# Kernel optimization log

Measured on AMD Instinct MI355X. Metric: run time of the kernel, lower is better.

Reference implementation:

```python
import jax, jax.numpy as jnp
import numpy as np
from jax.scipy.special import logsumexp

B, T, N = 512, 1024, 64


def setup_inputs() -> dict:
    key = jax.random.key(0)
    k1, k2, k3, k4, k5, k6 = jax.random.split(key, 6)
    emit = jax.random.normal(k1, (B, T, N), dtype=jnp.float32)
    target = jax.random.randint(k2, (B, T), 0, N)
    # valid monotone mask: each sequence has length in [T//2, T], length >= 1
    lengths = jax.random.randint(k3, (B,), T // 2, T + 1)
    mask = jnp.arange(T)[None, :] < lengths[:, None]  # [B, T] bool
    trans = 0.1 * jax.random.normal(k4, (N, N), dtype=jnp.float32)
    strans = 0.1 * jax.random.normal(k5, (N,), dtype=jnp.float32)
    etrans = 0.1 * jax.random.normal(k6, (N,), dtype=jnp.float32)
    return {"emit": emit, "target": target, "mask": mask,
            "trans": trans, "strans": strans, "etrans": etrans}


def _get_logZ(emit_t, mask_t, trans, strans, etrans):
    # emit_t: [T, B, N], mask_t: [T, B]
    alpha0 = strans[None, :] + emit_t[0]  # [B, N]

    def step(alpha, inp):
        e_i, m_i = inp  # [B, N], [B]
        # scores[b, j] = logsumexp_i(alpha[b, i] + trans[i, j] + e_i[b, j])
        scores = logsumexp(alpha[:, :, None] + trans[None, :, :], axis=1) + e_i
        alpha = jnp.where(m_i[:, None], scores, alpha)
        return alpha, None

    alpha, _ = jax.lax.scan(step, alpha0, (emit_t[1:], mask_t[1:]))
    logZ = logsumexp(alpha + etrans[None, :], axis=1).sum()
    return logZ / B


def _get_score(emit_t, target_t, mask_t, trans, strans, etrans):
    # emit_t: [T, B, N], target_t/mask_t: [T, B]
    emit_scores = jnp.take_along_axis(emit_t, target_t[:, :, None], axis=2)[:, :, 0]  # [T, B]
    trans_scores = trans[target_t[:-1], target_t[1:]]  # [T-1, B]
    scores = emit_scores.at[1:].add(trans_scores)
    score = jnp.where(mask_t, scores, 0.0).sum()
    ends = mask_t.sum(axis=0) - 1  # [B]
    score = score + strans[target_t[0]].sum()
    last_tags = target_t[ends, jnp.arange(target_t.shape[1])]
    score = score + etrans[last_tags].sum()
    return score / B


def reference(emit, target, mask, trans, strans, etrans):
    # batch_first=True -> move to time-major [T, B, ...]
    emit_t = jnp.swapaxes(emit, 0, 1)
    target_t = target.T
    mask_t = mask.T
    logZ = _get_logZ(emit_t, mask_t, trans, strans, etrans)
    score = _get_score(emit_t, target_t, mask_t, trans, strans, etrans)
    return logZ - score
```

## Files before the change

### kernel.cpp

```cpp
#include <hip/hip_runtime.h>

#define Bn 512
#define Tn 1024
#define Nn 64
#define BURN 16

typedef float    f4  __attribute__((ext_vector_type(4)));
typedef __fp16   pk2 __attribute__((ext_vector_type(2)));
typedef __fp16   pk4 __attribute__((ext_vector_type(4)));
typedef _Float16 h8v __attribute__((ext_vector_type(8)));

__device__ __forceinline__ float wave_sum(float v) {
#pragma unroll
    for (int off = 32; off >= 1; off >>= 1) v += __shfl_xor(v, off, 64);
    return v;
}

__global__ __launch_bounds__(64) void crf_mfma(
    const float* __restrict__ emit,
    const int*   __restrict__ target,
    const int*   __restrict__ mask,
    const float* __restrict__ trans,
    const float* __restrict__ strans,
    const float* __restrict__ etrans,
    float*       __restrict__ out)
{
    __shared__ __align__(16) _Float16 plds[16 * 72];

    const int lane = threadIdx.x;
    const int n = lane & 15;
    const int g = lane >> 4;
    const int b = blockIdx.x;
    const size_t ebase = (size_t)b * Tn * Nn;

    h8v A[4][2];
#pragma unroll
    for (int r = 0; r < 4; ++r)
#pragma unroll
        for (int h = 0; h < 2; ++h) {
            h8v a;
#pragma unroll
            for (int j = 0; j < 8; ++j)
                a[j] = (_Float16)__expf(trans[(32 * h + 8 * g + j) * Nn + 16 * r + n]);
            A[r][h] = a;
        }

    const int* mrow = mask + (size_t)b * Tn;
    int lsum = 0;
#pragma unroll
    for (int k = 0; k < Tn / Nn; ++k) lsum += mrow[k * Nn + lane];
#pragma unroll
    for (int off = 32; off >= 1; off >>= 1) lsum += __shfl_xor(lsum, off, 64);
    const int len = lsum;

    const int a0    = (n * len) >> 4;
    const int a1    = ((n + 1) * len) >> 4;
    const int start = n ? (a0 - BURN) : 1;
    const int tendv = a1 - 1;
    const int maxk  = ((len + 15) >> 4) + BURN;

    float wsel[4][4];
#pragma unroll
    for (int r = 0; r < 4; ++r) {
        f4 ee = *(const f4*)(emit + ebase + (size_t)(len - 1) * Nn + 16 * r + 4 * g);
        f4 et = *(const f4*)(etrans + 16 * r + 4 * g);
#pragma unroll
        for (int c = 0; c < 4; ++c)
            wsel[r][c] = (n == 15) ? __expf(ee[c] + et[c]) : 1.0f;
    }

    float U[4][4];
#pragma unroll
    for (int r = 0; r < 4; ++r) {
        f4 st = *(const f4*)(strans + 16 * r + 4 * g);
#pragma unroll
        for (int c = 0; c < 4; ++c)
            U[r][c] = (n == 0) ? __expf(st[c]) : 1.0f;
    }

    int   S = 0;
    float L0 = 0.0f, contrib = 0.0f;

    f4 rb[4];
    {
        const int tr = start - 1;
        const f4* p = (const f4*)(emit + ebase + (size_t)tr * Nn);
#pragma unroll
        for (int r = 0; r < 4; ++r) rb[r] = p[4 * r + g];
    }
    float Wx[4][4];
#pragma unroll
    for (int r = 0; r < 4; ++r)
#pragma unroll
        for (int c = 0; c < 4; ++c) Wx[r][c] = __expf(rb[r][c]);

    const f4 zero4 = {0.f, 0.f, 0.f, 0.f};
    _Float16* myCol = plds + n * 72;

    for (int k = 0; k < maxk; ++k) {
        {
            int tr = start + k;
            if (tr > Tn - 1) tr = Tn - 1;
            const f4* p = (const f4*)(emit + ebase + (size_t)tr * Nn);
#pragma unroll
            for (int r = 0; r < 4; ++r) rb[r] = p[4 * r + g];
        }

        if (k == BURN) {
            float cs = 0.f;
#pragma unroll
            for (int r = 0; r < 4; ++r)
#pragma unroll
                for (int c = 0; c < 4; ++c) cs += U[r][c];
            cs += __shfl_xor(cs, 16, 64);
            cs += __shfl_xor(cs, 32, 64);
            float l0v = __logf(cs);
            if (n) { L0 = l0v; S = 0; }
        }

        float mx = U[0][0];
#pragma unroll
        for (int r = 0; r < 4; ++r)
#pragma unroll
            for (int c = 0; c < 4; ++c) mx = fmaxf(mx, U[r][c]);
        mx = fmaxf(mx, __shfl_xor(mx, 16, 64));
        mx = fmaxf(mx, __shfl_xor(mx, 32, 64));
        const int mk = 127 - ((__float_as_int(mx) >> 23) & 0xff);
        S += mk;

#pragma unroll
        for (int r = 0; r < 4; ++r) {
            float p0 = U[r][0] * ldexpf(Wx[r][0], mk);
            float p1 = U[r][1] * ldexpf(Wx[r][1], mk);
            float p2 = U[r][2] * ldexpf(Wx[r][2], mk);
            float p3 = U[r][3] * ldexpf(Wx[r][3], mk);
            pk2 lo = __builtin_amdgcn_cvt_pkrtz(p0, p1);
            pk2 hi = __builtin_amdgcn_cvt_pkrtz(p2, p3);
            pk4 v4 = __builtin_shufflevector(lo, hi, 0, 1, 2, 3);
            *(pk4*)&myCol[16 * r + 4 * g] = v4;
        }

        h8v B0 = *(const h8v*)&myCol[8 * g];
        h8v B1 = *(const h8v*)&myCol[32 + 8 * g];

#pragma unroll
        for (int r = 0; r < 4; ++r) {
            f4 acc = __builtin_amdgcn_mfma_f32_16x16x32_f16(A[r][0], B0, zero4, 0, 0, 0);
            acc     = __builtin_amdgcn_mfma_f32_16x16x32_f16(A[r][1], B1, acc,   0, 0, 0);
#pragma unroll
            for (int c = 0; c < 4; ++c) U[r][c] = acc[c];
        }

        bool rec = (start + k) == tendv;
        if (__any(rec)) {
            float cs = 0.f;
#pragma unroll
            for (int r = 0; r < 4; ++r)
#pragma unroll
                for (int c = 0; c < 4; ++c) cs = fmaf(U[r][c], wsel[r][c], cs);
            cs += __shfl_xor(cs, 16, 64);
            cs += __shfl_xor(cs, 32, 64);
            float lv = __logf(cs);
            if (rec) contrib = lv - (float)S * 0.6931471805599453f - L0;
        }

#pragma unroll
        for (int r = 0; r < 4; ++r)
#pragma unroll
            for (int c = 0; c < 4; ++c) Wx[r][c] = __expf(rb[r][c]);
    }

    float tot = wave_sum(contrib) * 0.25f;

    const int* trow = target + (size_t)b * Tn;
    float sc = 0.0f;
#pragma unroll
    for (int k = 0; k < Tn / Nn; ++k) {
        int t = k * Nn + lane;
        if (t < len) {
            int gT = trow[t];
            sc += emit[ebase + (size_t)t * Nn + gT];
            if (t > 0) sc += trans[trow[t - 1] * Nn + gT];
        }
    }
    sc = wave_sum(sc);

    if (lane == 0) {
        sc += strans[trow[0]] + etrans[trow[len - 1]];
        atomicAdd(out, (tot - sc) * (1.0f / (float)Bn));
    }
}

extern "C" void kernel_launch(void* const* d_in, const int* in_sizes, int n_in,
                              void* d_out, int out_size, void* d_ws, size_t ws_size,
                              hipStream_t stream) {
    const float* emit   = (const float*)d_in[0];
    const int*   target = (const int*)d_in[1];
    const int*   mask   = (const int*)d_in[2];
    const float* trans  = (const float*)d_in[3];
    const float* strans = (const float*)d_in[4];
    const float* etrans = (const float*)d_in[5];
    float* out = (float*)d_out;

    (void)hipMemsetAsync(out, 0, sizeof(float), stream);
    crf_mfma<<<Bn, Nn, 0, stream>>>(emit, target, mask, trans, strans, etrans, out);
}
```

Measured before the change: 241.6 us.

## Feed MFMA B operand from registers and deepen emit prefetch ring

```diff
diff --git a/kernel.cpp b/kernel.cpp
--- a/kernel.cpp
+++ b/kernel.cpp
@@ -8,6 +8,7 @@
 typedef float    f4  __attribute__((ext_vector_type(4)));
 typedef __fp16   pk2 __attribute__((ext_vector_type(2)));
 typedef __fp16   pk4 __attribute__((ext_vector_type(4)));
+typedef __fp16   pk8 __attribute__((ext_vector_type(8)));
 typedef _Float16 h8v __attribute__((ext_vector_type(8)));
 
 __device__ __forceinline__ float wave_sum(float v) {
@@ -25,8 +26,6 @@
     const float* __restrict__ etrans,
     float*       __restrict__ out)
 {
-    __shared__ __align__(16) _Float16 plds[16 * 72];
-
     const int lane = threadIdx.x;
     const int n = lane & 15;
     const int g = lane >> 4;
@@ -40,8 +39,10 @@
         for (int h = 0; h < 2; ++h) {
             h8v a;
 #pragma unroll
-            for (int j = 0; j < 8; ++j)
-                a[j] = (_Float16)__expf(trans[(32 * h + 8 * g + j) * Nn + 16 * r + n]);
+            for (int j = 0; j < 8; ++j) {
+                int kk = 32 * h + 16 * (j >> 2) + 4 * g + (j & 3);
+                a[j] = (_Float16)__expf(trans[kk * Nn + 16 * r + n]);
+            }
             A[r][h] = a;
         }
 
@@ -81,93 +82,102 @@
     int   S = 0;
     float L0 = 0.0f, contrib = 0.0f;
 
-    f4 rb[4];
-    {
-        const int tr = start - 1;
+    f4 rbuf[8][4];
+#pragma unroll
+    for (int d = 0; d < 8; ++d) {
+        int tr = start - 1 + d; if (tr > Tn - 1) tr = Tn - 1;
         const f4* p = (const f4*)(emit + ebase + (size_t)tr * Nn);
 #pragma unroll
-        for (int r = 0; r < 4; ++r) rb[r] = p[4 * r + g];
-    }
-    float Wx[4][4];
-#pragma unroll
-    for (int r = 0; r < 4; ++r)
-#pragma unroll
-        for (int c = 0; c < 4; ++c) Wx[r][c] = __expf(rb[r][c]);
+        for (int r = 0; r < 4; ++r) rbuf[d][r] = p[4 * r + g];
+    }
 
     const f4 zero4 = {0.f, 0.f, 0.f, 0.f};
-    _Float16* myCol = plds + n * 72;
-
-    for (int k = 0; k < maxk; ++k) {
-        {
-            int tr = start + k;
-            if (tr > Tn - 1) tr = Tn - 1;
-            const f4* p = (const f4*)(emit + ebase + (size_t)tr * Nn);
-#pragma unroll
-            for (int r = 0; r < 4; ++r) rb[r] = p[4 * r + g];
+    const int nkb = (maxk + 7) >> 3;
+
+    for (int kb = 0; kb < nkb; ++kb) {
+#pragma unroll
+        for (int q = 0; q < 8; ++q) {
+            const int k = 8 * kb + q;
+
+            float Wx[4][4];
+#pragma unroll
+            for (int r = 0; r < 4; ++r)
+#pragma unroll
+                for (int c = 0; c < 4; ++c) Wx[r][c] = __expf(rbuf[q][r][c]);
+            {
+                int tr = start + k + 7; if (tr > Tn - 1) tr = Tn - 1;
+                const f4* p = (const f4*)(emit + ebase + (size_t)tr * Nn);
+#pragma unroll
+                for (int r = 0; r < 4; ++r) rbuf[q][r] = p[4 * r + g];
+            }
+
+            if (k == BURN) {
+                float cs = 0.f;
+#pragma unroll
+                for (int r = 0; r < 4; ++r)
+#pragma unroll
+                    for (int c = 0; c < 4; ++c) cs += U[r][c];
+                cs += __shfl_xor(cs, 16, 64);
+                cs += __shfl_xor(cs, 32, 64);
+                float l0v = __logf(cs);
+                if (n) { L0 = l0v; S = 0; }
+            }
+
+            float m0 = fmaxf(fmaxf(U[0][0], U[0][1]), fmaxf(U[0][2], U[0][3]));
+            float m1 = fmaxf(fmaxf(U[1][0], U[1][1]), fmaxf(U[1][2], U[1][3]));
+            float m2 = fmaxf(fmaxf(U[2][0], U[2][1]), fmaxf(U[2][2], U[2][3]));
+            float m3 = fmaxf(fmaxf(U[3][0], U[3][1]), fmaxf(U[3][2], U[3][3]));
+            float mx = fmaxf(fmaxf(m0, m1), fmaxf(m2, m3));
+            mx = fmaxf(mx, __shfl_xor(mx, 16, 64));
+            mx = fmaxf(mx, __shfl_xor(mx, 32, 64));
+            const int mk = 127 - ((__float_as_int(mx) >> 23) & 0xff);
+            S += mk;
+            const float sc2 = __int_as_float((127 + mk) << 23);
+
+            float P_[4][4];
+#pragma unroll
+            for (int r = 0; r < 4; ++r)
+#pragma unroll
+                for (int c = 0; c < 4; ++c) P_[r][c] = U[r][c] * sc2 * Wx[r][c];
+
+            pk2 c00 = __builtin_amdgcn_cvt_pkrtz(P_[0][0], P_[0][1]);
+            pk2 c01 = __builtin_amdgcn_cvt_pkrtz(P_[0][2], P_[0][3]);
+            pk2 c10 = __builtin_amdgcn_cvt_pkrtz(P_[1][0], P_[1][1]);
+            pk2 c11 = __builtin_amdgcn_cvt_pkrtz(P_[1][2], P_[1][3]);
+            pk2 c20 = __builtin_amdgcn_cvt_pkrtz(P_[2][0], P_[2][1]);
+            pk2 c21 = __builtin_amdgcn_cvt_pkrtz(P_[2][2], P_[2][3]);
+            pk2 c30 = __builtin_amdgcn_cvt_pkrtz(P_[3][0], P_[3][1]);
+            pk2 c31 = __builtin_amdgcn_cvt_pkrtz(P_[3][2], P_[3][3]);
+            pk4 b0lo = __builtin_shufflevector(c00, c01, 0, 1, 2, 3);
+            pk4 b0hi = __builtin_shufflevector(c10, c11, 0, 1, 2, 3);
+            pk4 b1lo = __builtin_shufflevector(c20, c21, 0, 1, 2, 3);
+            pk4 b1hi = __builtin_shufflevector(c30, c31, 0, 1, 2, 3);
+            pk8 b0p = __builtin_shufflevector(b0lo, b0hi, 0, 1, 2, 3, 4, 5, 6, 7);
+            pk8 b1p = __builtin_shufflevector(b1lo, b1hi, 0, 1, 2, 3, 4, 5, 6, 7);
+            h8v B0 = __builtin_bit_cast(h8v, b0p);
+            h8v B1 = __builtin_bit_cast(h8v, b1p);
+
+#pragma unroll
+            for (int r = 0; r < 4; ++r) {
+                f4 acc = __builtin_amdgcn_mfma_f32_16x16x32_f16(A[r][0], B0, zero4, 0, 0, 0);
+                acc     = __builtin_amdgcn_mfma_f32_16x16x32_f16(A[r][1], B1, acc,   0, 0, 0);
+#pragma unroll
+                for (int c = 0; c < 4; ++c) U[r][c] = acc[c];
+            }
+
+            bool rec = (start + k) == tendv;
+            if (__any(rec)) {
+                float cs = 0.f;
+#pragma unroll
+                for (int r = 0; r < 4; ++r)
+#pragma unroll
+                    for (int c = 0; c < 4; ++c) cs = fmaf(U[r][c], wsel[r][c], cs);
+                cs += __shfl_xor(cs, 16, 64);
+                cs += __shfl_xor(cs, 32, 64);
+                float lv = __logf(cs);
+                if (rec) contrib = lv - (float)S * 0.6931471805599453f - L0;
+            }
         }
-
-        if (k == BURN) {
-            float cs = 0.f;
-#pragma unroll
-            for (int r = 0; r < 4; ++r)
-#pragma unroll
-                for (int c = 0; c < 4; ++c) cs += U[r][c];
-            cs += __shfl_xor(cs, 16, 64);
-            cs += __shfl_xor(cs, 32, 64);
-            float l0v = __logf(cs);
-            if (n) { L0 = l0v; S = 0; }
-        }
-
-        float mx = U[0][0];
-#pragma unroll
-        for (int r = 0; r < 4; ++r)
-#pragma unroll
-            for (int c = 0; c < 4; ++c) mx = fmaxf(mx, U[r][c]);
-        mx = fmaxf(mx, __shfl_xor(mx, 16, 64));
-        mx = fmaxf(mx, __shfl_xor(mx, 32, 64));
-        const int mk = 127 - ((__float_as_int(mx) >> 23) & 0xff);
-        S += mk;
-
-#pragma unroll
-        for (int r = 0; r < 4; ++r) {
-            float p0 = U[r][0] * ldexpf(Wx[r][0], mk);
-            float p1 = U[r][1] * ldexpf(Wx[r][1], mk);
-            float p2 = U[r][2] * ldexpf(Wx[r][2], mk);
-            float p3 = U[r][3] * ldexpf(Wx[r][3], mk);
-            pk2 lo = __builtin_amdgcn_cvt_pkrtz(p0, p1);
-            pk2 hi = __builtin_amdgcn_cvt_pkrtz(p2, p3);
-            pk4 v4 = __builtin_shufflevector(lo, hi, 0, 1, 2, 3);
-            *(pk4*)&myCol[16 * r + 4 * g] = v4;
-        }
-
-        h8v B0 = *(const h8v*)&myCol[8 * g];
-        h8v B1 = *(const h8v*)&myCol[32 + 8 * g];
-
-#pragma unroll
-        for (int r = 0; r < 4; ++r) {
-            f4 acc = __builtin_amdgcn_mfma_f32_16x16x32_f16(A[r][0], B0, zero4, 0, 0, 0);
-            acc     = __builtin_amdgcn_mfma_f32_16x16x32_f16(A[r][1], B1, acc,   0, 0, 0);
-#pragma unroll
-            for (int c = 0; c < 4; ++c) U[r][c] = acc[c];
-        }
-
-        bool rec = (start + k) == tendv;
-        if (__any(rec)) {
-            float cs = 0.f;
-#pragma unroll
-            for (int r = 0; r < 4; ++r)
-#pragma unroll
-                for (int c = 0; c < 4; ++c) cs = fmaf(U[r][c], wsel[r][c], cs);
-            cs += __shfl_xor(cs, 16, 64);
-            cs += __shfl_xor(cs, 32, 64);
-            float lv = __logf(cs);
-            if (rec) contrib = lv - (float)S * 0.6931471805599453f - L0;
-        }
-
-#pragma unroll
-        for (int r = 0; r < 4; ++r)
-#pragma unroll
-            for (int c = 0; c < 4; ++c) Wx[r][c] = __expf(rb[r][c]);
     }
 
     float tot = wave_sum(contrib) * 0.25f;
```

Result: faster. 223.9 us (-7.4%).
